# Optimization experiments

Measured on AMD Instinct MI355X. Metric: run time of the kernel, lower is better.

The kernel has to match this reference:

```python
import jax, jax.numpy as jnp
import numpy as np

BN_EPS = 1e-5


def _conv(x, w):
    # x: [N, Cin, H, W], w: [Cout, Cin, kh, kw], stride 1, padding 1 (same for 3x3)
    return jax.lax.conv_general_dilated(
        x, w, window_strides=(1, 1), padding=[(1, 1), (1, 1)],
        dimension_numbers=('NCHW', 'OIHW', 'NCHW'))


def setup_inputs() -> dict:
    key = jax.random.key(0)
    ks = jax.random.split(key, 4)
    T, N, Cin, Cout, H, W = 16, 4, 64, 64, 64, 64
    x = jax.random.normal(ks[0], (T, N, Cin, H, W), dtype=jnp.float32)
    # conv_x2h: Conv2d(Cin, 4*Cout, k=3, s=1, p=1, bias=True) + BatchNorm2d(4*Cout)
    Wx = jax.random.normal(ks[1], (4 * Cout, Cin, 3, 3), dtype=jnp.float32) * 0.05
    bx = jax.random.normal(ks[2], (4 * Cout,), dtype=jnp.float32) * 0.05
    gamma = jnp.ones((4 * Cout,), dtype=jnp.float32)
    beta = jnp.zeros((4 * Cout,), dtype=jnp.float32)
    # conv_h2h: Conv2d(Cout, 4*Cout, k=3, p=1, bias=False)
    Wh = jax.random.normal(ks[3], (4 * Cout, Cout, 3, 3), dtype=jnp.float32) * 0.05
    return {"x": x, "Wx": Wx, "bx": bx, "gamma": gamma, "beta": beta, "Wh": Wh}


def reference(x, Wx, bx, gamma, beta, Wh):
    T, N, Cin, H, W = x.shape
    hidden = Wh.shape[1]

    # ---- SequenceWise(Conv2d + BatchNorm(train) + Identity) ----
    xf = x.reshape(T * N, Cin, H, W)
    y = _conv(xf, Wx) + bx[None, :, None, None]
    mean = jnp.mean(y, axis=(0, 2, 3))
    var = jnp.var(y, axis=(0, 2, 3))  # biased, as torch BN uses for normalization
    y = (y - mean[None, :, None, None]) * jax.lax.rsqrt(var[None, :, None, None] + BN_EPS)
    y = y * gamma[None, :, None, None] + beta[None, :, None, None]
    y = y.reshape(T, N, 4 * hidden, H, W)

    # ---- ConvLSTMCell recurrence over time ----
    # zeros init is exactly equivalent to prev_h/prev_c = None:
    # conv_h2h(0) = 0 (no bias) and f*0 + i*g = i*g.
    h0 = jnp.zeros((N, hidden, H, W), dtype=x.dtype)
    c0 = jnp.zeros((N, hidden, H, W), dtype=x.dtype)

    def step(carry, xt):
        h, c = carry
        tmp = _conv(h, Wh) + xt
        cc_i, cc_f, cc_o, cc_g = jnp.split(tmp, 4, axis=1)
        i = jax.nn.sigmoid(cc_i)
        f = jax.nn.sigmoid(cc_f)
        o = jax.nn.sigmoid(cc_o)
        g = jnp.tanh(cc_g)
        c = f * c + i * g
        h = o * jnp.tanh(c)
        return (h, c), h

    _, hs = jax.lax.scan(step, (h0, c0), y)
    return hs  # [T, N, hidden, H, W]
```

## Files before the change

### kernel.cpp

```cpp
#include <hip/hip_runtime.h>
#include <hip/hip_bf16.h>

typedef float        f32x4  __attribute__((ext_vector_type(4)));
typedef unsigned int u32x4  __attribute__((ext_vector_type(4)));
typedef __bf16       bf16x8 __attribute__((ext_vector_type(8)));

__device__ __forceinline__ unsigned short f2bf(float f) {
    unsigned u = __builtin_bit_cast(unsigned, f);
    u += 0x7fffu + ((u >> 16) & 1u);
    return (unsigned short)(u >> 16);
}
__device__ __forceinline__ float bf2f(unsigned short u) {
    union { unsigned ui; float f; } c; c.ui = ((unsigned)u) << 16; return c.f;
}

__global__ __launch_bounds__(256) void k_xT(const float* __restrict__ x,
                                            unsigned short* __restrict__ xT) {
    int bid = blockIdx.x;
    int img = bid >> 4;
    int p   = (bid & 15) * 256 + threadIdx.x;
    const float* xi = x + (size_t)img * 64 * 4096 + p;
    unsigned short r[64];
#pragma unroll
    for (int ci = 0; ci < 64; ++ci) r[ci] = f2bf(xi[(size_t)ci * 4096]);
    u32x4* dst = (u32x4*)(xT + ((size_t)img * 4096 + p) * 64);
#pragma unroll
    for (int c8 = 0; c8 < 8; ++c8) dst[c8] = *(u32x4*)&r[c8 * 8];
}

__global__ __launch_bounds__(256) void k_pack(const float* __restrict__ W,
                                              unsigned short* __restrict__ Ap,
                                              int gatePerm) {
    int idx = blockIdx.x * 256 + threadIdx.x;
    if (idx >= 256 * 576) return;
    int row = idx / 576, k = idx % 576;
    int tap = k / 64, cil = k % 64;
    int kb = cil >> 5, w32 = cil & 31;
    int s = w32 >> 3, e = w32 & 7;
    int ci = kb * 32 + ((s ^ (row & 3)) << 3) + e;
    int co = gatePerm ? ((row & 3) * 64 + (row >> 2)) : row;
    Ap[idx] = f2bf(W[((size_t)co * 64 + ci) * 9 + tap]);
}

template<int MODE>
__global__ __launch_bounds__(256) void k_conv(
    const unsigned short* __restrict__ src,
    const unsigned short* __restrict__ Ap,
    unsigned short* __restrict__ ybf,
    const float* __restrict__ ss,
    float* __restrict__ cst,
    unsigned short* __restrict__ hout,
    float* __restrict__ out,
    float2* __restrict__ prt,
    int t, int first)
{
    constexpr int TH    = MODE ? 8 : 16;
    constexpr int N_    = MODE ? 2 : 4;
    constexpr int HR    = TH + 2;
    constexpr int TMSK  = MODE ? 31 : 15;
    constexpr int IMGSH = MODE ? 7 : 6;

    __shared__ __align__(16) unsigned short halo[HR * 18 * 32];
    __shared__ __align__(16) unsigned short As[2][64 * 32];

    const int bid  = blockIdx.x;
    const int grp  = bid & 3;
    const int tile = (bid >> 2) & TMSK;
    const int img  = bid >> IMGSH;
    const int py0 = (tile >> 2) * TH, px0 = (tile & 3) * 16;
    const int tid = threadIdx.x;
    const int wv = tid >> 6, lane = tid & 63;
    const int cl = lane & 15, q = lane >> 4;
    const int rowbase = grp * 64;

    f32x4 acc[4][N_];
#pragma unroll
    for (int m = 0; m < 4; ++m)
#pragma unroll
        for (int n = 0; n < N_; ++n)
            acc[m][n] = (f32x4){0.f, 0.f, 0.f, 0.f};

    const bool skip = (MODE == 1) && first;

    if (!skip) {
        const unsigned short* sb = src + (size_t)img * 4096 * 64;
        char* hB = (char*)halo;
        auto stage_halo = [&](int ch2) {
            for (int tau = tid; tau < HR * 72; tau += 256) {
                int s = tau & 3, hcc = (tau >> 2) % 18, hrr = tau / 72;
                int gy = py0 + hrr - 1, gx = px0 + hcc - 1;
                u32x4 v = {0u, 0u, 0u, 0u};
                if ((unsigned)gy < 64u && (unsigned)gx < 64u)
                    v = *(const u32x4*)(sb + ((gy * 64 + gx) * 64 + ch2 * 32 + s * 8));
                *(u32x4*)(hB + (hrr * 18 + hcc) * 64 + ((s * 16) ^ ((hcc & 3) << 4))) = v;
            }
        };
        const char* agp = (const char*)Ap +
            (size_t)(rowbase + (tid >> 2)) * 1152 + (tid & 3) * 16;
        char* AsWr = (char*)(&As[0][0]) + (tid >> 2) * 64 + (tid & 3) * 16;
        *(u32x4*)AsWr = *(const u32x4*)agp;
        stage_halo(0);
        __syncthreads();

        int aoff[4];
#pragma unroll
        for (int m = 0; m < 4; ++m)
            aoff[m] = (m * 16 + cl) * 64 + ((q * 16) ^ ((cl & 3) << 4));

        const char* AsRd = (const char*)(&As[0][0]);
        int buf = 0;
        for (int ks = 0; ks < 18; ++ks) {
            int tap = ks % 9;
            int ky = tap / 3, kx = tap - ky * 3;
            bool have = ks < 17;
            u32x4 an;
            if (have) {
                int ksn = ks + 1, tapn = ksn % 9, ch2n = ksn / 9;
                an = *(const u32x4*)(agp + tapn * 128 + ch2n * 64);
            }
            u32x4 af[4];
#pragma unroll
            for (int m = 0; m < 4; ++m)
                af[m] = *(const u32x4*)(AsRd + buf * 4096 + aoff[m]);

            int hcv  = cl + kx;
            int cbase = hcv * 64 + ((q * 16) ^ ((hcv & 3) << 4));
#pragma unroll
            for (int n = 0; n < N_; ++n) {
                int hr = wv * N_ + n + ky;
                u32x4 bv = *(const u32x4*)(hB + hr * 1152 + cbase);
                bf16x8 bfr = __builtin_bit_cast(bf16x8, bv);
#pragma unroll
                for (int m = 0; m < 4; ++m)
                    acc[m][n] = __builtin_amdgcn_mfma_f32_16x16x32_bf16(
                        __builtin_bit_cast(bf16x8, af[m]), bfr, acc[m][n], 0, 0, 0);
            }
            if (have) *(u32x4*)(AsWr + ((buf ^ 1) << 12)) = an;
            if (ks == 8) {
                __syncthreads();
                stage_halo(1);
            }
            __syncthreads();
            buf ^= 1;
        }
    }

    if (MODE == 0) {
#pragma unroll
        for (int m = 0; m < 4; ++m) {
            int co = rowbase + m * 16 + q * 4;
#pragma unroll
            for (int n = 0; n < N_; ++n) {
                int pix = (py0 + wv * N_ + n) * 64 + px0 + cl;
                unsigned short* yp = ybf + (size_t)img * 256 * 4096 + pix;
#pragma unroll
                for (int j = 0; j < 4; ++j)
                    yp[(size_t)(co + j) * 4096] = f2bf(acc[m][n][j]);
            }
        }
        float* bnred = (float*)&As[0][0];
#pragma unroll
        for (int m = 0; m < 4; ++m) {
#pragma unroll
            for (int j = 0; j < 4; ++j) {
                float s = 0.f, qq = 0.f;
#pragma unroll
                for (int n = 0; n < N_; ++n) {
                    float v = acc[m][n][j];
                    s += v; qq += v * v;
                }
#pragma unroll
                for (int mask = 1; mask <= 8; mask <<= 1) {
                    s  += __shfl_xor(s,  mask, 64);
                    qq += __shfl_xor(qq, mask, 64);
                }
                if (cl == 0) {
                    int ci_ = (wv * 4 + q) * 16 + m * 4 + j;
                    bnred[ci_ * 2]     = s;
                    bnred[ci_ * 2 + 1] = qq;
                }
            }
        }
        __syncthreads();
        if (tid < 64) {
            int m_ = tid >> 4, qj = tid & 15;
            float s = 0.f, qq = 0.f;
#pragma unroll
            for (int w = 0; w < 4; ++w) {
                int idx = ((w * 4 + (qj >> 2)) * 16 + m_ * 4 + (qj & 3)) * 2;
                s += bnred[idx]; qq += bnred[idx + 1];
            }
            prt[(size_t)(rowbase + tid) * 1024 + img * 16 + tile] = make_float2(s, qq);
        }
    } else {
        unsigned short* hbounce = &As[0][0];
        __syncthreads();
#pragma unroll
        for (int m = 0; m < 4; ++m) {
            int hc = grp * 16 + m * 4 + q;
            float sc[4], sh[4];
#pragma unroll
            for (int j = 0; j < 4; ++j) {
                sc[j] = ss[j * 64 + hc];
                sh[j] = ss[256 + j * 64 + hc];
            }
#pragma unroll
            for (int n = 0; n < N_; ++n) {
                int pix = (py0 + wv * N_ + n) * 64 + px0 + cl;
                float tmp[4];
#pragma unroll
                for (int j = 0; j < 4; ++j) {
                    float yv = bf2f(ybf[((size_t)((t * 4 + img) * 256 + j * 64 + hc)) * 4096 + pix]);
                    tmp[j] = acc[m][n][j] + sc[j] * yv + sh[j];
                }
                float iv = 1.f / (1.f + __expf(-tmp[0]));
                float fv = 1.f / (1.f + __expf(-tmp[1]));
                float ov = 1.f / (1.f + __expf(-tmp[2]));
                float e2 = __expf(2.f * tmp[3]);
                float gv = 1.f - 2.f / (e2 + 1.f);
                size_t cidx = ((size_t)img * 64 + hc) * 4096 + pix;
                float cnew = fv * cst[cidx] + iv * gv;
                cst[cidx] = cnew;
                float e2c = __expf(2.f * cnew);
                float hv  = ov * (1.f - 2.f / (e2c + 1.f));
                out[((size_t)(t * 4 + img) * 64 + hc) * 4096 + pix] = hv;
                hbounce[((wv * N_ + n) * 16 + cl) * 16 + m * 4 + q] = f2bf(hv);
            }
        }
        __syncthreads();
        if (tid < TH * 16) {
            int pixg = (py0 + (tid >> 4)) * 64 + px0 + (tid & 15);
            u32x4* dst = (u32x4*)(hout + ((size_t)img * 4096 + pixg) * 64 + grp * 16);
            u32x4* s0  = (u32x4*)(hbounce + tid * 16);
            dst[0] = s0[0];
            dst[1] = s0[1];
        }
    }
}

__global__ __launch_bounds__(256) void k_bn_fin(
    const float2* __restrict__ prt, const float* __restrict__ bx,
    const float* __restrict__ gamma, const float* __restrict__ beta,
    float* __restrict__ ss) {
    int c = blockIdx.x;
    const float2* p = prt + (size_t)c * 1024;
    float s = 0.f, sq = 0.f;
    for (int i = threadIdx.x; i < 1024; i += 256) {
        float2 v = p[i]; s += v.x; sq += v.y;
    }
    __shared__ float rs[256], rq[256];
    int tid = threadIdx.x;
    rs[tid] = s; rq[tid] = sq;
    __syncthreads();
    for (int off = 128; off > 0; off >>= 1) {
        if (tid < off) { rs[tid] += rs[tid + off]; rq[tid] += rq[tid + off]; }
        __syncthreads();
    }
    if (tid == 0) {
        float mean = rs[0] * (1.f / 262144.f);
        float var  = rq[0] * (1.f / 262144.f) - mean * mean;
        float sc   = gamma[c] * rsqrtf(var + 1e-5f);
        ss[c]       = sc;
        ss[256 + c] = beta[c] - mean * sc;
        (void)bx;
    }
}

extern "C" void kernel_launch(void* const* d_in, const int* in_sizes, int n_in,
                              void* d_out, int out_size, void* d_ws, size_t ws_size,
                              hipStream_t stream) {
    const float* x     = (const float*)d_in[0];
    const float* Wx    = (const float*)d_in[1];
    const float* bx    = (const float*)d_in[2];
    const float* gamma = (const float*)d_in[3];
    const float* beta  = (const float*)d_in[4];
    const float* Wh    = (const float*)d_in[5];
    float* out = (float*)d_out;

    char* ws = (char*)d_ws;
    unsigned short* y   = (unsigned short*)ws;
    unsigned short* Axp = (unsigned short*)(ws + 134217728);
    unsigned short* Ahp = (unsigned short*)(ws + 134512640);
    float*          ss  = (float*)(ws + 134807552);
    float*          cs  = (float*)(ws + 134809600);
    float2*         prt = (float2*)(ws + 139003904);
    unsigned short* hA  = (unsigned short*)(ws + 139003904);
    unsigned short* hB  = (unsigned short*)(ws + 141101056);

    unsigned short* xT = (unsigned short*)d_out;

    k_xT  <<<1024, 256, 0, stream>>>(x, xT);
    k_pack<<< 576, 256, 0, stream>>>(Wx, Axp, 0);
    k_pack<<< 576, 256, 0, stream>>>(Wh, Ahp, 1);
    hipMemsetAsync(cs, 0, 4194304, stream);

    k_conv<0><<<4096, 256, 0, stream>>>(xT, Axp, y, nullptr, nullptr, nullptr,
                                        nullptr, prt, 0, 0);
    k_bn_fin<<<256, 256, 0, stream>>>(prt, bx, gamma, beta, ss);

    unsigned short* hbuf[2] = {hA, hB};
    for (int t = 0; t < 16; ++t) {
        k_conv<1><<<512, 256, 0, stream>>>(hbuf[t & 1], Ahp, y, ss, cs,
                                           hbuf[(t + 1) & 1], out, nullptr,
                                           t, t == 0 ? 1 : 0);
    }
}
```

Before: 432.9 us.

## Stage full 64-channel halo once and load weights directly into registers

The conv kernel now stages all 64 input channels of the halo tile into shared memory in one pass instead of two 32-channel halves. It drops the double-buffered shared A tile and instead prefetches the weight fragments straight from global memory into registers, with the packed weight layout reordered to match. This removes the per-k-step __syncthreads and the mid-loop restage barrier. In exchange it uses more shared memory for the halo and issues redundant per-lane global (L2/L1) weight loads.

```diff
diff --git a/kernel.cpp b/kernel.cpp
--- a/kernel.cpp
+++ b/kernel.cpp
@@ -34,10 +34,9 @@
     int idx = blockIdx.x * 256 + threadIdx.x;
     if (idx >= 256 * 576) return;
     int row = idx / 576, k = idx % 576;
-    int tap = k / 64, cil = k % 64;
-    int kb = cil >> 5, w32 = cil & 31;
-    int s = w32 >> 3, e = w32 & 7;
-    int ci = kb * 32 + ((s ^ (row & 3)) << 3) + e;
+    int ks = k / 32, c32 = k % 32;
+    int half = ks / 9, tap = ks % 9;
+    int ci = half * 32 + c32;
     int co = gatePerm ? ((row & 3) * 64 + (row >> 2)) : row;
     Ap[idx] = f2bf(W[((size_t)co * 64 + ci) * 9 + tap]);
 }
@@ -60,8 +59,7 @@
     constexpr int TMSK  = MODE ? 31 : 15;
     constexpr int IMGSH = MODE ? 7 : 6;
 
-    __shared__ __align__(16) unsigned short halo[HR * 18 * 32];
-    __shared__ __align__(16) unsigned short As[2][64 * 32];
+    __shared__ __align__(16) unsigned short halo[HR * 18 * 64];
 
     const int bid  = blockIdx.x;
     const int grp  = bid & 3;
@@ -85,63 +83,45 @@
     if (!skip) {
         const unsigned short* sb = src + (size_t)img * 4096 * 64;
         char* hB = (char*)halo;
-        auto stage_halo = [&](int ch2) {
-            for (int tau = tid; tau < HR * 72; tau += 256) {
-                int s = tau & 3, hcc = (tau >> 2) % 18, hrr = tau / 72;
-                int gy = py0 + hrr - 1, gx = px0 + hcc - 1;
-                u32x4 v = {0u, 0u, 0u, 0u};
-                if ((unsigned)gy < 64u && (unsigned)gx < 64u)
-                    v = *(const u32x4*)(sb + ((gy * 64 + gx) * 64 + ch2 * 32 + s * 8));
-                *(u32x4*)(hB + (hrr * 18 + hcc) * 64 + ((s * 16) ^ ((hcc & 3) << 4))) = v;
-            }
-        };
-        const char* agp = (const char*)Ap +
-            (size_t)(rowbase + (tid >> 2)) * 1152 + (tid & 3) * 16;
-        char* AsWr = (char*)(&As[0][0]) + (tid >> 2) * 64 + (tid & 3) * 16;
-        *(u32x4*)AsWr = *(const u32x4*)agp;
-        stage_halo(0);
-        __syncthreads();
-
-        int aoff[4];
+        for (int tau = tid; tau < HR * 144; tau += 256) {
+            int s = tau & 7, hcc = (tau >> 3) % 18, hrr = tau / 144;
+            int gy = py0 + hrr - 1, gx = px0 + hcc - 1;
+            u32x4 v = {0u, 0u, 0u, 0u};
+            if ((unsigned)gy < 64u && (unsigned)gx < 64u)
+                v = *(const u32x4*)(sb + ((gy * 64 + gx) * 64 + s * 8));
+            *(u32x4*)(hB + (hrr * 18 + hcc) * 128 + ((s * 16) ^ ((hcc & 7) << 4))) = v;
+        }
+        __syncthreads();
+
+        const char* Apb = (const char*)Ap + (size_t)(rowbase + cl) * 1152 + q * 16;
+
+        u32x4 af[4], afn[4];
 #pragma unroll
         for (int m = 0; m < 4; ++m)
-            aoff[m] = (m * 16 + cl) * 64 + ((q * 16) ^ ((cl & 3) << 4));
-
-        const char* AsRd = (const char*)(&As[0][0]);
-        int buf = 0;
+            af[m] = *(const u32x4*)(Apb + m * 18432);
+
         for (int ks = 0; ks < 18; ++ks) {
-            int tap = ks % 9;
+            if (ks < 17) {
+#pragma unroll
+                for (int m = 0; m < 4; ++m)
+                    afn[m] = *(const u32x4*)(Apb + m * 18432 + (ks + 1) * 64);
+            }
+            int tap = ks % 9, kb = ks / 9;
             int ky = tap / 3, kx = tap - ky * 3;
-            bool have = ks < 17;
-            u32x4 an;
-            if (have) {
-                int ksn = ks + 1, tapn = ksn % 9, ch2n = ksn / 9;
-                an = *(const u32x4*)(agp + tapn * 128 + ch2n * 64);
-            }
-            u32x4 af[4];
-#pragma unroll
-            for (int m = 0; m < 4; ++m)
-                af[m] = *(const u32x4*)(AsRd + buf * 4096 + aoff[m]);
-
             int hcv  = cl + kx;
-            int cbase = hcv * 64 + ((q * 16) ^ ((hcv & 3) << 4));
+            int cbase = hcv * 128 + ((kb * 64 + q * 16) ^ ((hcv & 7) << 4));
 #pragma unroll
             for (int n = 0; n < N_; ++n) {
                 int hr = wv * N_ + n + ky;
-                u32x4 bv = *(const u32x4*)(hB + hr * 1152 + cbase);
+                u32x4 bv = *(const u32x4*)(hB + hr * 2304 + cbase);
                 bf16x8 bfr = __builtin_bit_cast(bf16x8, bv);
 #pragma unroll
                 for (int m = 0; m < 4; ++m)
                     acc[m][n] = __builtin_amdgcn_mfma_f32_16x16x32_bf16(
                         __builtin_bit_cast(bf16x8, af[m]), bfr, acc[m][n], 0, 0, 0);
             }
-            if (have) *(u32x4*)(AsWr + ((buf ^ 1) << 12)) = an;
-            if (ks == 8) {
-                __syncthreads();
-                stage_halo(1);
-            }
-            __syncthreads();
-            buf ^= 1;
+#pragma unroll
+            for (int m = 0; m < 4; ++m) af[m] = afn[m];
         }
     }
 
@@ -158,7 +138,8 @@
                     yp[(size_t)(co + j) * 4096] = f2bf(acc[m][n][j]);
             }
         }
-        float* bnred = (float*)&As[0][0];
+        __syncthreads();
+        float* bnred = (float*)halo;
 #pragma unroll
         for (int m = 0; m < 4; ++m) {
 #pragma unroll
@@ -193,7 +174,7 @@
             prt[(size_t)(rowbase + tid) * 1024 + img * 16 + tile] = make_float2(s, qq);
         }
     } else {
-        unsigned short* hbounce = &As[0][0];
+        unsigned short* hbounce = halo;
         __syncthreads();
 #pragma unroll
         for (int m = 0; m < 4; ++m) {
```

Result: slower. 604.2 us (+39.6%).
